# Kernel optimization log

Hardware: AMD Instinct MI355X
Metric: run time of the kernel (lower is better)

## Reference

```python
import jax, jax.numpy as jnp
import numpy as np

COMMITMENT_COST = 0.25
NUM_EMBEDDINGS = 512
EMBEDDING_DIM = 64


def setup_inputs() -> dict:
    key = jax.random.key(0)
    k1, k2 = jax.random.split(key)
    inputs = jax.random.normal(k1, (64, EMBEDDING_DIM, 32, 32), dtype=jnp.float32)
    # nn.Embedding init: uniform(-1/K, 1/K)
    emb_w = jax.random.uniform(
        k2, (NUM_EMBEDDINGS, EMBEDDING_DIM), dtype=jnp.float32,
        minval=-1.0 / NUM_EMBEDDINGS, maxval=1.0 / NUM_EMBEDDINGS)
    return {"inputs": inputs, "emb_w": emb_w}


def reference(inputs, emb_w):
    sg = jax.lax.stop_gradient
    # NCHW -> NHWC
    x = jnp.transpose(inputs, (0, 2, 3, 1))          # [B, H, W, D]
    B, H, W, D = x.shape
    flat = x.reshape(-1, D)                          # [N, D]
    dist = (jnp.sum(flat * flat, axis=1, keepdims=True)
            + jnp.sum(emb_w * emb_w, axis=1)
            - 2.0 * jnp.dot(flat, emb_w.T))          # [N, K]
    idx = jnp.argmin(dist, axis=1)                   # [N]
    # one-hot @ emb_w is just a gather
    quantized = emb_w[idx].reshape(B, H, W, D)       # [B, H, W, D]
    e_latent_loss = jnp.mean((sg(quantized) - x) ** 2)
    q_latent_loss = jnp.mean((quantized - sg(x)) ** 2)
    loss = q_latent_loss + COMMITMENT_COST * e_latent_loss
    # straight-through estimator
    quantized_st = x + sg(quantized - x)
    out = jnp.transpose(quantized_st, (0, 3, 1, 2))  # back to NCHW
    return loss, out, idx[:, None]
```

## Files before the change

### kernel.cpp

```cpp
#include <hip/hip_runtime.h>


#define D_    64
#define HW_   1024
#define N_    65536
#define K_    512
#define M_    128
#define CH_   128
#define NCH_  4
#define NDTOT (N_ * D_)

__global__ __launch_bounds__(256) void vq_norm_kernel(const float* __restrict__ emb,
                                                      float* __restrict__ wsn) {
    int k = blockIdx.x * 256 + threadIdx.x;
    if (k < K_) {
        const float* e = emb + k * D_;
        float r[8];
#pragma unroll
        for (int j = 0; j < 8; ++j) r[j] = __fmul_rn(e[j], e[j]);
#pragma unroll
        for (int i = 1; i < 8; ++i)
#pragma unroll
            for (int j = 0; j < 8; ++j)
                r[j] = __fadd_rn(r[j], __fmul_rn(e[i * 8 + j], e[i * 8 + j]));
        float s = __fadd_rn(__fadd_rn(__fadd_rn(r[0], r[1]), __fadd_rn(r[2], r[3])),
                            __fadd_rn(__fadd_rn(r[4], r[5]), __fadd_rn(r[6], r[7])));
        wsn[k] = s;
    }
}

__global__ __launch_bounds__(256, 2) void vq_main_kernel(const float* __restrict__ inp,
                                                         const float* __restrict__ emb,
                                                         const float* __restrict__ wsn,
                                                         float* __restrict__ out) {
    __shared__ float lds[16520];
    float* ldsx = lds;
    float* ldse = lds + 8192;
    float* sxs  = lds + 16384;
    float* partial = lds + 16512;

    const int tid = threadIdx.x;
    const int pg  = tid & 15;
    const int kg  = tid >> 4;
    const int n0  = blockIdx.x * M_;
    const int b   = n0 >> 10;
    const int hw0 = n0 & 1023;
    const float* xbase = inp + b * (D_ * HW_) + hw0;

#pragma unroll
    for (int i = 0; i < 8; ++i) {
        int q  = i * 256 + tid;
        int d  = q >> 5;
        int pq = q & 31;
        float4 v = *(const float4*)(xbase + d * HW_ + pq * 4);
        *(float4*)(ldsx + d * M_ + pq * 4) = v;
    }
    __syncthreads();

    if (tid < M_) {
        float r[8];
#pragma unroll
        for (int j = 0; j < 8; ++j) {
            float v = ldsx[j * M_ + tid];
            r[j] = __fmul_rn(v, v);
        }
#pragma unroll
        for (int i = 1; i < 8; ++i)
#pragma unroll
            for (int j = 0; j < 8; ++j) {
                float v = ldsx[(i * 8 + j) * M_ + tid];
                r[j] = __fadd_rn(r[j], __fmul_rn(v, v));
            }
        sxs[tid] = __fadd_rn(__fadd_rn(__fadd_rn(r[0], r[1]), __fadd_rn(r[2], r[3])),
                             __fadd_rn(__fadd_rn(r[4], r[5]), __fadd_rn(r[6], r[7])));
    }
    __syncthreads();

    float sxp[8];
#pragma unroll
    for (int pp = 0; pp < 8; ++pp) sxp[pp] = sxs[pg * 8 + pp];

    float runv[8];
    int   runi[8];
#pragma unroll
    for (int pp = 0; pp < 8; ++pp) { runv[pp] = 3.4e38f; runi[pp] = 0; }

    for (int c = 0; c < NCH_; ++c) {
        __syncthreads();
#pragma unroll
        for (int i = 0; i < 8; ++i) {
            int q  = i * 256 + tid;
            int kl = q & 127;
            int dq = q >> 7;
            float4 v = *(const float4*)(emb + (c * CH_ + kl) * D_ + dq * 4);
            ldse[(dq * 4 + 0) * CH_ + kl] = v.x;
            ldse[(dq * 4 + 1) * CH_ + kl] = v.y;
            ldse[(dq * 4 + 2) * CH_ + kl] = v.z;
            ldse[(dq * 4 + 3) * CH_ + kl] = v.w;
        }
        float4 nh0 = *(const float4*)(wsn + c * CH_ + kg * 8);
        float4 nh1 = *(const float4*)(wsn + c * CH_ + kg * 8 + 4);
        __syncthreads();

        float acc[8][8];
#pragma unroll
        for (int pp = 0; pp < 8; ++pp)
#pragma unroll
            for (int kk = 0; kk < 8; ++kk) acc[pp][kk] = 0.f;

#pragma unroll 2
        for (int d = 0; d < D_; ++d) {
            float4 xa = *(const float4*)(ldsx + d * M_ + pg * 8);
            float4 xb = *(const float4*)(ldsx + d * M_ + pg * 8 + 4);
            float4 ea = *(const float4*)(ldse + d * CH_ + kg * 8);
            float4 eb = *(const float4*)(ldse + d * CH_ + kg * 8 + 4);
            float xr[8] = {xa.x, xa.y, xa.z, xa.w, xb.x, xb.y, xb.z, xb.w};
            float er[8] = {ea.x, ea.y, ea.z, ea.w, eb.x, eb.y, eb.z, eb.w};
#pragma unroll
            for (int pp = 0; pp < 8; ++pp)
#pragma unroll
                for (int kk = 0; kk < 8; ++kk)
                    acc[pp][kk] = fmaf(xr[pp], er[kk], acc[pp][kk]);
        }

        float nk[8] = {nh0.x, nh0.y, nh0.z, nh0.w, nh1.x, nh1.y, nh1.z, nh1.w};
#pragma unroll
        for (int pp = 0; pp < 8; ++pp) {
            float sx = sxp[pp];
#pragma unroll
            for (int kk = 0; kk < 8; ++kk) {
                float t1 = __fadd_rn(sx, nk[kk]);
                float v  = __fadd_rn(t1, -2.0f * acc[pp][kk]);
                if (v < runv[pp]) { runv[pp] = v; runi[pp] = c * CH_ + kg * 8 + kk; }
            }
        }
    }

    __syncthreads();
    float* sv = ldse;
    int*   si = (int*)(ldse + 2048);
    int*   fi = (int*)(ldse + 4096);
#pragma unroll
    for (int pp = 0; pp < 8; ++pp) {
        sv[kg * M_ + pg * 8 + pp] = runv[pp];
        si[kg * M_ + pg * 8 + pp] = runi[pp];
    }
    __syncthreads();
    if (tid < M_) {
        float bv = 3.4e38f; int bi = 0x7fffffff;
#pragma unroll
        for (int g = 0; g < 16; ++g) {
            float v  = sv[g * M_ + tid];
            int   ii = si[g * M_ + tid];
            if (v < bv || (v == bv && ii < bi)) { bv = v; bi = ii; }
        }
        fi[tid] = bi;
        out[1 + NDTOT + n0 + tid] = (float)bi;
    }
    __syncthreads();

    float* obase = out + 1 + b * (D_ * HW_) + hw0;
    float local = 0.f;
    for (int i = 0; i < 32; ++i) {
        int q = i * 256 + tid;
        int d = q >> 7;
        int p = q & 127;
        int idx = fi[p];
        float e  = emb[idx * D_ + d];
        float xv = ldsx[d * M_ + p];
        float df = e - xv;
        local = fmaf(df, df, local);
        obase[d * HW_ + p] = e;
    }
#pragma unroll
    for (int off = 32; off > 0; off >>= 1)
        local += __shfl_down(local, off, 64);
    if ((tid & 63) == 0) partial[tid >> 6] = local;
    __syncthreads();
    if (tid == 0) {
        float t = partial[0] + partial[1] + partial[2] + partial[3];
        atomicAdd(out, t * (1.25f / (float)NDTOT));
    }
}

extern "C" void kernel_launch(void* const* d_in, const int* in_sizes, int n_in,
                              void* d_out, int out_size, void* d_ws, size_t ws_size,
                              hipStream_t stream) {
    const float* inp = (const float*)d_in[0];
    const float* emb = (const float*)d_in[1];
    float* out = (float*)d_out;
    float* wsn = (float*)d_ws;

    hipMemsetAsync(d_out, 0, sizeof(float), stream);
    vq_norm_kernel<<<2, 256, 0, stream>>>(emb, wsn);
    vq_main_kernel<<<512, 256, 0, stream>>>(inp, emb, wsn, out);
}
```

Before: 132.1 us.

## Replace LDS-tiled register-blocked distance GEMM with per-thread register x and wave-uniform codebook reads

The main kernel drops the LDS tiling of inputs and codebook chunks with 8x8 register blocking. Each thread now holds one pixel's 64-dim vector in registers. Each wave scans 128 codes, reading embedding rows through wave-uniform (scalar) loads, and blocks handle 64 pixels with 1024 blocks in total. The goal is to remove LDS traffic and barriers and to raise occupancy. The cost is much less data reuse per FMA: one FMA per scalar-loaded element. The tie-break on equal distances also changes, and the distance now uses an fmaf, which can alter rounding compared with the reference.

```diff
diff --git a/kernel.cpp b/kernel.cpp
--- a/kernel.cpp
+++ b/kernel.cpp
@@ -5,10 +5,9 @@
 #define HW_   1024
 #define N_    65536
 #define K_    512
-#define M_    128
-#define CH_   128
-#define NCH_  4
-#define NDTOT (N_ * D_)
+#define NDTOT 4194304
+#define PB_   64
+#define KW_   128
 
 __global__ __launch_bounds__(256) void vq_norm_kernel(const float* __restrict__ emb,
                                                       float* __restrict__ wsn) {
@@ -23,163 +22,95 @@
 #pragma unroll
             for (int j = 0; j < 8; ++j)
                 r[j] = __fadd_rn(r[j], __fmul_rn(e[i * 8 + j], e[i * 8 + j]));
-        float s = __fadd_rn(__fadd_rn(__fadd_rn(r[0], r[1]), __fadd_rn(r[2], r[3])),
-                            __fadd_rn(__fadd_rn(r[4], r[5]), __fadd_rn(r[6], r[7])));
-        wsn[k] = s;
+        wsn[k] = __fadd_rn(__fadd_rn(__fadd_rn(r[0], r[1]), __fadd_rn(r[2], r[3])),
+                           __fadd_rn(__fadd_rn(r[4], r[5]), __fadd_rn(r[6], r[7])));
     }
 }
 
-__global__ __launch_bounds__(256, 2) void vq_main_kernel(const float* __restrict__ inp,
+__global__ __launch_bounds__(256, 4) void vq_main_kernel(const float* __restrict__ inp,
                                                          const float* __restrict__ emb,
                                                          const float* __restrict__ wsn,
                                                          float* __restrict__ out) {
-    __shared__ float lds[16520];
-    float* ldsx = lds;
-    float* ldse = lds + 8192;
-    float* sxs  = lds + 16384;
-    float* partial = lds + 16512;
+    __shared__ float sv[4][PB_];
+    __shared__ int   si[4][PB_];
+    __shared__ int   fi[PB_];
 
-    const int tid = threadIdx.x;
-    const int pg  = tid & 15;
-    const int kg  = tid >> 4;
-    const int n0  = blockIdx.x * M_;
+    const int tid  = threadIdx.x;
+    const int lane = tid & 63;
+    const int wv   = __builtin_amdgcn_readfirstlane(tid >> 6);
+
+    const int n0  = blockIdx.x * PB_;
     const int b   = n0 >> 10;
     const int hw0 = n0 & 1023;
-    const float* xbase = inp + b * (D_ * HW_) + hw0;
+    const float* xcol = inp + b * (D_ * HW_) + hw0 + lane;
 
+    float x[64];
 #pragma unroll
-    for (int i = 0; i < 8; ++i) {
-        int q  = i * 256 + tid;
-        int d  = q >> 5;
-        int pq = q & 31;
-        float4 v = *(const float4*)(xbase + d * HW_ + pq * 4);
-        *(float4*)(ldsx + d * M_ + pq * 4) = v;
+    for (int d = 0; d < D_; ++d) x[d] = xcol[d * HW_];
+
+    float r[8];
+#pragma unroll
+    for (int j = 0; j < 8; ++j) r[j] = __fmul_rn(x[j], x[j]);
+#pragma unroll
+    for (int i = 1; i < 8; ++i)
+#pragma unroll
+        for (int j = 0; j < 8; ++j)
+            r[j] = __fadd_rn(r[j], __fmul_rn(x[i * 8 + j], x[i * 8 + j]));
+    const float sx = __fadd_rn(__fadd_rn(__fadd_rn(r[0], r[1]), __fadd_rn(r[2], r[3])),
+                               __fadd_rn(__fadd_rn(r[4], r[5]), __fadd_rn(r[6], r[7])));
+
+    float runv = 3.4e38f;
+    int   runi = 0;
+    const int k0 = wv * KW_;
+    for (int kk = 0; kk < KW_; ++kk) {
+        const int k = k0 + kk;
+        const float* e = emb + k * D_;
+        float acc = 0.f;
+#pragma unroll
+        for (int d = 0; d < D_; ++d)
+            acc = fmaf(x[d], e[d], acc);
+        float t1 = __fadd_rn(sx, wsn[k]);
+        float v  = fmaf(-2.0f, acc, t1);
+        if (v < runv) { runv = v; runi = k; }
     }
+    sv[wv][lane] = runv;
+    si[wv][lane] = runi;
     __syncthreads();
 
-    if (tid < M_) {
-        float r[8];
+    if (tid < PB_) {
+        float bv = 3.4e38f; int bi = 0;
 #pragma unroll
-        for (int j = 0; j < 8; ++j) {
-            float v = ldsx[j * M_ + tid];
-            r[j] = __fmul_rn(v, v);
-        }
-#pragma unroll
-        for (int i = 1; i < 8; ++i)
-#pragma unroll
-            for (int j = 0; j < 8; ++j) {
-                float v = ldsx[(i * 8 + j) * M_ + tid];
-                r[j] = __fadd_rn(r[j], __fmul_rn(v, v));
-            }
-        sxs[tid] = __fadd_rn(__fadd_rn(__fadd_rn(r[0], r[1]), __fadd_rn(r[2], r[3])),
-                             __fadd_rn(__fadd_rn(r[4], r[5]), __fadd_rn(r[6], r[7])));
-    }
-    __syncthreads();
-
-    float sxp[8];
-#pragma unroll
-    for (int pp = 0; pp < 8; ++pp) sxp[pp] = sxs[pg * 8 + pp];
-
-    float runv[8];
-    int   runi[8];
-#pragma unroll
-    for (int pp = 0; pp < 8; ++pp) { runv[pp] = 3.4e38f; runi[pp] = 0; }
-
-    for (int c = 0; c < NCH_; ++c) {
-        __syncthreads();
-#pragma unroll
-        for (int i = 0; i < 8; ++i) {
-            int q  = i * 256 + tid;
-            int kl = q & 127;
-            int dq = q >> 7;
-            float4 v = *(const float4*)(emb + (c * CH_ + kl) * D_ + dq * 4);
-            ldse[(dq * 4 + 0) * CH_ + kl] = v.x;
-            ldse[(dq * 4 + 1) * CH_ + kl] = v.y;
-            ldse[(dq * 4 + 2) * CH_ + kl] = v.z;
-            ldse[(dq * 4 + 3) * CH_ + kl] = v.w;
-        }
-        float4 nh0 = *(const float4*)(wsn + c * CH_ + kg * 8);
-        float4 nh1 = *(const float4*)(wsn + c * CH_ + kg * 8 + 4);
-        __syncthreads();
-
-        float acc[8][8];
-#pragma unroll
-        for (int pp = 0; pp < 8; ++pp)
-#pragma unroll
-            for (int kk = 0; kk < 8; ++kk) acc[pp][kk] = 0.f;
-
-#pragma unroll 2
-        for (int d = 0; d < D_; ++d) {
-            float4 xa = *(const float4*)(ldsx + d * M_ + pg * 8);
-            float4 xb = *(const float4*)(ldsx + d * M_ + pg * 8 + 4);
-            float4 ea = *(const float4*)(ldse + d * CH_ + kg * 8);
-            float4 eb = *(const float4*)(ldse + d * CH_ + kg * 8 + 4);
-            float xr[8] = {xa.x, xa.y, xa.z, xa.w, xb.x, xb.y, xb.z, xb.w};
-            float er[8] = {ea.x, ea.y, ea.z, ea.w, eb.x, eb.y, eb.z, eb.w};
-#pragma unroll
-            for (int pp = 0; pp < 8; ++pp)
-#pragma unroll
-                for (int kk = 0; kk < 8; ++kk)
-                    acc[pp][kk] = fmaf(xr[pp], er[kk], acc[pp][kk]);
-        }
-
-        float nk[8] = {nh0.x, nh0.y, nh0.z, nh0.w, nh1.x, nh1.y, nh1.z, nh1.w};
-#pragma unroll
-        for (int pp = 0; pp < 8; ++pp) {
-            float sx = sxp[pp];
-#pragma unroll
-            for (int kk = 0; kk < 8; ++kk) {
-                float t1 = __fadd_rn(sx, nk[kk]);
-                float v  = __fadd_rn(t1, -2.0f * acc[pp][kk]);
-                if (v < runv[pp]) { runv[pp] = v; runi[pp] = c * CH_ + kg * 8 + kk; }
-            }
-        }
-    }
-
-    __syncthreads();
-    float* sv = ldse;
-    int*   si = (int*)(ldse + 2048);
-    int*   fi = (int*)(ldse + 4096);
-#pragma unroll
-    for (int pp = 0; pp < 8; ++pp) {
-        sv[kg * M_ + pg * 8 + pp] = runv[pp];
-        si[kg * M_ + pg * 8 + pp] = runi[pp];
-    }
-    __syncthreads();
-    if (tid < M_) {
-        float bv = 3.4e38f; int bi = 0x7fffffff;
-#pragma unroll
-        for (int g = 0; g < 16; ++g) {
-            float v  = sv[g * M_ + tid];
-            int   ii = si[g * M_ + tid];
-            if (v < bv || (v == bv && ii < bi)) { bv = v; bi = ii; }
+        for (int g = 0; g < 4; ++g) {
+            float v  = sv[g][tid];
+            int   ii = si[g][tid];
+            if (v < bv) { bv = v; bi = ii; }
         }
         fi[tid] = bi;
         out[1 + NDTOT + n0 + tid] = (float)bi;
     }
     __syncthreads();
 
-    float* obase = out + 1 + b * (D_ * HW_) + hw0;
-    float local = 0.f;
-    for (int i = 0; i < 32; ++i) {
-        int q = i * 256 + tid;
-        int d = q >> 7;
-        int p = q & 127;
-        int idx = fi[p];
-        float e  = emb[idx * D_ + d];
-        float xv = ldsx[d * M_ + p];
-        float df = e - xv;
-        local = fmaf(df, df, local);
-        obase[d * HW_ + p] = e;
-    }
+    if (wv == 0) {
+        const int idx = fi[lane];
+        const float4* erow = (const float4*)(emb + idx * D_);
+        float* ob = out + 1 + b * (D_ * HW_) + hw0 + lane;
+        float local = 0.f;
 #pragma unroll
-    for (int off = 32; off > 0; off >>= 1)
-        local += __shfl_down(local, off, 64);
-    if ((tid & 63) == 0) partial[tid >> 6] = local;
-    __syncthreads();
-    if (tid == 0) {
-        float t = partial[0] + partial[1] + partial[2] + partial[3];
-        atomicAdd(out, t * (1.25f / (float)NDTOT));
+        for (int j = 0; j < 16; ++j) {
+            float4 e4 = erow[j];
+            float ev[4] = {e4.x, e4.y, e4.z, e4.w};
+#pragma unroll
+            for (int c = 0; c < 4; ++c) {
+                float df = ev[c] - x[j * 4 + c];
+                local = fmaf(df, df, local);
+                ob[(j * 4 + c) * HW_] = ev[c];
+            }
+        }
+#pragma unroll
+        for (int off = 32; off > 0; off >>= 1)
+            local += __shfl_down(local, off, 64);
+        if (lane == 0)
+            atomicAdd(out, local * (1.25f / (float)NDTOT));
     }
 }
 
@@ -193,5 +124,5 @@
 
     hipMemsetAsync(d_out, 0, sizeof(float), stream);
     vq_norm_kernel<<<2, 256, 0, stream>>>(emb, wsn);
-    vq_main_kernel<<<512, 256, 0, stream>>>(inp, emb, wsn, out);
+    vq_main_kernel<<<N_ / PB_, 256, 0, stream>>>(inp, emb, wsn, out);
 }
```

New measurement: 151.0 us. 14.3% more time.
